# Performance work log

Measured on AMD Instinct MI355X. Metric: run time of the kernel, lower is better.

## Reference

```python
import jax, jax.numpy as jnp
import numpy as np

B, S, IN, OUT = 4, 2048, 4096, 4096

def setup_inputs() -> dict:
    key = jax.random.key(0)
    k1, k2, k3, k4 = jax.random.split(key, 4)
    x = jax.random.normal(k1, (B, S, IN), dtype=jnp.float32)
    # sign is mathematically +/-1 (sign of original fp weights)
    sign = jnp.sign(jax.random.normal(k2, (OUT, IN), dtype=jnp.float32))
    # per-row scale = mean(|W|), strictly positive
    scale = jax.random.uniform(k3, (OUT,), dtype=jnp.float32, minval=1e-3, maxval=0.1)
    bias = jax.random.normal(k4, (OUT,), dtype=jnp.float32)
    return {"x": x, "sign": sign, "scale": scale, "bias": bias}

def reference(x, sign, scale, bias) -> jnp.ndarray:
    # y = (x @ sign.T) * scale + bias  -- W approx diag(scale) * sign(W_orig)
    y = jnp.einsum('bsi,oi->bso', x, sign)
    return y * scale + bias
```

## Files before the change

### kernel.cpp

```cpp
#include <hip/hip_runtime.h>

#define M_DIM 8192
#define N_DIM 4096
#define K_DIM 4096
#define BK 32
#define NT (K_DIM / BK)

typedef __attribute__((ext_vector_type(8))) short bf16x8;
typedef __attribute__((ext_vector_type(8))) unsigned short u16x8;
typedef __attribute__((ext_vector_type(4))) float f32x4;

__device__ inline unsigned short f32_to_bf16_rne(float f) {
  unsigned int u = __float_as_uint(f);
  u += 0x7FFFu + ((u >> 16) & 1u);
  return (unsigned short)(u >> 16);
}

__global__ __launch_bounds__(256) void cvt_f32_bf16_kernel(
    const float* __restrict__ in, unsigned short* __restrict__ out) {
  const int i = (blockIdx.x * 256 + threadIdx.x) * 8;
  float4 v0 = *(const float4*)(in + i);
  float4 v1 = *(const float4*)(in + i + 4);
  u16x8 o;
  o[0] = f32_to_bf16_rne(v0.x);
  o[1] = f32_to_bf16_rne(v0.y);
  o[2] = f32_to_bf16_rne(v0.z);
  o[3] = f32_to_bf16_rne(v0.w);
  o[4] = f32_to_bf16_rne(v1.x);
  o[5] = f32_to_bf16_rne(v1.y);
  o[6] = f32_to_bf16_rne(v1.z);
  o[7] = f32_to_bf16_rne(v1.w);
  *(u16x8*)(out + i) = o;
}

__device__ inline void gld_lds16(const void* g, void* l) {
  __builtin_amdgcn_global_load_lds(
      (__attribute__((address_space(1))) void*)(g),
      (__attribute__((address_space(3))) void*)(l),
      16, 0, 0);
}

__global__ __launch_bounds__(512, 2) void gemm_sign_kernel(
    const unsigned short* __restrict__ A,
    const unsigned short* __restrict__ Bm,
    const float* __restrict__ scale,
    const float* __restrict__ bias,
    float* __restrict__ C) {
  __shared__ __align__(16) unsigned short smA[4][256 * BK];
  __shared__ __align__(16) unsigned short smB[4][256 * BK];

  const int tid   = threadIdx.x;
  const int lane  = tid & 63;
  const int wave  = tid >> 6;
  const int waveM = wave >> 2;
  const int waveN = wave & 3;
  const int lrow  = lane & 15;

  const int bid   = blockIdx.x;
  const int wgid  = (bid & 7) * 64 + (bid >> 3);
  const int mBase = (wgid >> 4) * 256;
  const int nBase = (wgid & 15) * 256;

  const int srow = tid >> 2;
  const int gcol = ((tid & 3) ^ ((tid >> 3) & 3)) * 8;
  const unsigned short* aSrc = A  + (size_t)(mBase + srow) * K_DIM + gcol;
  const unsigned short* bSrc = Bm + (size_t)(nBase + srow) * K_DIM + gcol;
  const size_t rowStr128 = (size_t)128 * K_DIM;

#define STAGE_A(buf, kt) do {                                        \
    const unsigned short* _s = aSrc + (size_t)(kt) * BK;             \
    gld_lds16(_s,             &smA[buf][tid * 8]);                   \
    gld_lds16(_s + rowStr128, &smA[buf][4096 + tid * 8]);            \
  } while (0)
#define STAGE_B(buf, kt) do {                                        \
    const unsigned short* _s = bSrc + (size_t)(kt) * BK;             \
    gld_lds16(_s,             &smB[buf][tid * 8]);                   \
    gld_lds16(_s + rowStr128, &smB[buf][4096 + tid * 8]);            \
  } while (0)

  const int cSwz = ((lane >> 4) ^ ((lrow >> 1) & 3)) * 8;
  int aOff[8], bOff[4];
#pragma unroll
  for (int mi = 0; mi < 8; ++mi)
    aOff[mi] = (waveM * 128 + mi * 16 + lrow) * BK + cSwz;
#pragma unroll
  for (int ni = 0; ni < 4; ++ni)
    bOff[ni] = (waveN * 64 + ni * 16 + lrow) * BK + cSwz;

  f32x4 acc[8][4];
#pragma unroll
  for (int i = 0; i < 8; ++i)
#pragma unroll
    for (int j = 0; j < 4; ++j)
      acc[i][j] = (f32x4){0.f, 0.f, 0.f, 0.f};

  STAGE_A(0, 0); STAGE_B(0, 0);
  STAGE_A(1, 1); STAGE_B(1, 1);
  asm volatile("s_waitcnt vmcnt(4)" ::: "memory");
  __builtin_amdgcn_s_barrier();

#pragma unroll 4
  for (int t = 0; t < NT; ++t) {
    const int cur = t & 3;
    const int pre = (t + 2) & 3;
    const int kt2 = (t + 2 < NT) ? (t + 2) : (NT - 1);
    bf16x8 af[4], bf[4];

#pragma unroll
    for (int ni = 0; ni < 4; ++ni)
      bf[ni] = *(const bf16x8*)&smB[cur][bOff[ni]];
#pragma unroll
    for (int mi = 0; mi < 4; ++mi)
      af[mi] = *(const bf16x8*)&smA[cur][aOff[mi]];
    STAGE_A(pre, kt2);
    __builtin_amdgcn_s_barrier();
    asm volatile("s_waitcnt lgkmcnt(0)" ::: "memory");
    __builtin_amdgcn_s_setprio(1);
#pragma unroll
    for (int mi = 0; mi < 4; ++mi)
#pragma unroll
      for (int ni = 0; ni < 4; ++ni)
        acc[mi][ni] = __builtin_amdgcn_mfma_f32_16x16x32_bf16(
            af[mi], bf[ni], acc[mi][ni], 0, 0, 0);
    __builtin_amdgcn_s_setprio(0);
    __builtin_amdgcn_s_barrier();

#pragma unroll
    for (int mi = 0; mi < 4; ++mi)
      af[mi] = *(const bf16x8*)&smA[cur][aOff[4 + mi]];
    STAGE_B(pre, kt2);
    asm volatile("s_waitcnt vmcnt(4)" ::: "memory");
    __builtin_amdgcn_s_barrier();
    asm volatile("s_waitcnt lgkmcnt(0)" ::: "memory");
    __builtin_amdgcn_s_setprio(1);
#pragma unroll
    for (int mi = 0; mi < 4; ++mi)
#pragma unroll
      for (int ni = 0; ni < 4; ++ni)
        acc[4 + mi][ni] = __builtin_amdgcn_mfma_f32_16x16x32_bf16(
            af[mi], bf[ni], acc[4 + mi][ni], 0, 0, 0);
    __builtin_amdgcn_s_setprio(0);
    __builtin_amdgcn_s_barrier();
  }
#undef STAGE_A
#undef STAGE_B

#pragma unroll
  for (int ni = 0; ni < 4; ++ni) {
    const int c = nBase + waveN * 64 + ni * 16 + lrow;
    const float sc = scale[c];
    const float bs = bias[c];
#pragma unroll
    for (int mi = 0; mi < 8; ++mi) {
      const int r0 = mBase + waveM * 128 + mi * 16 + (lane >> 4) * 4;
#pragma unroll
      for (int r = 0; r < 4; ++r)
        C[(size_t)(r0 + r) * N_DIM + c] = acc[mi][ni][r] * sc + bs;
    }
  }
}

extern "C" void kernel_launch(void* const* d_in, const int* in_sizes, int n_in,
                              void* d_out, int out_size, void* d_ws, size_t ws_size,
                              hipStream_t stream) {
  const float* x     = (const float*)d_in[0];
  const float* sign  = (const float*)d_in[1];
  const float* scale = (const float*)d_in[2];
  const float* bias  = (const float*)d_in[3];
  float* out = (float*)d_out;

  unsigned short* xb    = (unsigned short*)d_ws;
  unsigned short* signb = xb + (size_t)M_DIM * K_DIM;

  cvt_f32_bf16_kernel<<<(M_DIM * K_DIM) / 2048, 256, 0, stream>>>(x, xb);
  cvt_f32_bf16_kernel<<<(N_DIM * K_DIM) / 2048, 256, 0, stream>>>(sign, signb);

  gemm_sign_kernel<<<dim3(512), dim3(512), 0, stream>>>(xb, signb, scale, bias, out);
}
```

Measured before the change: 527.3 us.

## Deepen GEMM pipeline: prefetch three tiles and software-pipeline LDS fragment reads

The global-to-LDS prefetch distance goes from two to three K-tiles across the 4-slot ring. The main loop is software-pipelined so the next tile's A and B register fragments are read from LDS during the current tile's second MFMA half, using ping-pong B registers and partial lgkmcnt waits. The aim is to overlap LDS read latency and global load latency with MFMA work and to drop one barrier per half-step. In exchange it needs more registers and depends on delicate waitcnt and barrier ordering, where a mistake would cause a race.

```diff
diff --git a/kernel.cpp b/kernel.cpp
--- a/kernel.cpp
+++ b/kernel.cpp
@@ -94,54 +94,70 @@
     for (int j = 0; j < 4; ++j)
       acc[i][j] = (f32x4){0.f, 0.f, 0.f, 0.f};
 
+  bf16x8 afP[4], afQ[4], bfE[4], bfO[4];
+
   STAGE_A(0, 0); STAGE_B(0, 0);
   STAGE_A(1, 1); STAGE_B(1, 1);
+  STAGE_A(2, 2); STAGE_B(2, 2);
   asm volatile("s_waitcnt vmcnt(4)" ::: "memory");
   __builtin_amdgcn_s_barrier();
+#pragma unroll
+  for (int ni = 0; ni < 4; ++ni)
+    bfE[ni] = *(const bf16x8*)&smB[0][bOff[ni]];
+#pragma unroll
+  for (int mi = 0; mi < 4; ++mi)
+    afP[mi] = *(const bf16x8*)&smA[0][aOff[mi]];
 
-#pragma unroll 4
-  for (int t = 0; t < NT; ++t) {
-    const int cur = t & 3;
-    const int pre = (t + 2) & 3;
-    const int kt2 = (t + 2 < NT) ? (t + 2) : (NT - 1);
-    bf16x8 af[4], bf[4];
+#define TILE_BODY(t, bfC, bfN)                                          \
+  {                                                                     \
+    const int cur = (t) & 3;                                            \
+    const int pre = ((t) + 3) & 3;                                      \
+    const int kt3 = ((t) + 3 < NT) ? ((t) + 3) : (NT - 1);              \
+    const int ktn = ((t) + 1 < NT) ? ((t) + 1) : (NT - 1);              \
+    const int nxt = ktn & 3;                                            \
+        \
+    \
+    _Pragma("unroll")                                                   \
+    for (int mi = 0; mi < 4; ++mi)                                      \
+      afQ[mi] = *(const bf16x8*)&smA[cur][aOff[4 + mi]];                \
+    STAGE_A(pre, kt3);                                                  \
+    asm volatile("s_waitcnt lgkmcnt(4)" ::: "memory");                  \
+    __builtin_amdgcn_s_setprio(1);                                      \
+    _Pragma("unroll")                                                   \
+    for (int mi = 0; mi < 4; ++mi)                                      \
+      _Pragma("unroll")                                                 \
+      for (int ni = 0; ni < 4; ++ni)                                    \
+        acc[mi][ni] = __builtin_amdgcn_mfma_f32_16x16x32_bf16(          \
+            afP[mi], bfC[ni], acc[mi][ni], 0, 0, 0);                    \
+    __builtin_amdgcn_s_setprio(0);                                      \
+    __builtin_amdgcn_s_barrier();                                       \
+       \
+       \
+    _Pragma("unroll")                                                   \
+    for (int ni = 0; ni < 4; ++ni)                                      \
+      bfN[ni] = *(const bf16x8*)&smB[nxt][bOff[ni]];                    \
+    _Pragma("unroll")                                                   \
+    for (int mi = 0; mi < 4; ++mi)                                      \
+      afP[mi] = *(const bf16x8*)&smA[nxt][aOff[mi]];                    \
+    STAGE_B(pre, kt3);                                                  \
+    asm volatile("s_waitcnt lgkmcnt(8)" ::: "memory");                  \
+    __builtin_amdgcn_s_setprio(1);                                      \
+    _Pragma("unroll")                                                   \
+    for (int mi = 0; mi < 4; ++mi)                                      \
+      _Pragma("unroll")                                                 \
+      for (int ni = 0; ni < 4; ++ni)                                    \
+        acc[4 + mi][ni] = __builtin_amdgcn_mfma_f32_16x16x32_bf16(      \
+            afQ[mi], bfC[ni], acc[4 + mi][ni], 0, 0, 0);                \
+    __builtin_amdgcn_s_setprio(0);                                      \
+    asm volatile("s_waitcnt vmcnt(4)" ::: "memory");                    \
+    __builtin_amdgcn_s_barrier();                                       \
+  }
 
-#pragma unroll
-    for (int ni = 0; ni < 4; ++ni)
-      bf[ni] = *(const bf16x8*)&smB[cur][bOff[ni]];
-#pragma unroll
-    for (int mi = 0; mi < 4; ++mi)
-      af[mi] = *(const bf16x8*)&smA[cur][aOff[mi]];
-    STAGE_A(pre, kt2);
-    __builtin_amdgcn_s_barrier();
-    asm volatile("s_waitcnt lgkmcnt(0)" ::: "memory");
-    __builtin_amdgcn_s_setprio(1);
-#pragma unroll
-    for (int mi = 0; mi < 4; ++mi)
-#pragma unroll
-      for (int ni = 0; ni < 4; ++ni)
-        acc[mi][ni] = __builtin_amdgcn_mfma_f32_16x16x32_bf16(
-            af[mi], bf[ni], acc[mi][ni], 0, 0, 0);
-    __builtin_amdgcn_s_setprio(0);
-    __builtin_amdgcn_s_barrier();
-
-#pragma unroll
-    for (int mi = 0; mi < 4; ++mi)
-      af[mi] = *(const bf16x8*)&smA[cur][aOff[4 + mi]];
-    STAGE_B(pre, kt2);
-    asm volatile("s_waitcnt vmcnt(4)" ::: "memory");
-    __builtin_amdgcn_s_barrier();
-    asm volatile("s_waitcnt lgkmcnt(0)" ::: "memory");
-    __builtin_amdgcn_s_setprio(1);
-#pragma unroll
-    for (int mi = 0; mi < 4; ++mi)
-#pragma unroll
-      for (int ni = 0; ni < 4; ++ni)
-        acc[4 + mi][ni] = __builtin_amdgcn_mfma_f32_16x16x32_bf16(
-            af[mi], bf[ni], acc[4 + mi][ni], 0, 0, 0);
-    __builtin_amdgcn_s_setprio(0);
-    __builtin_amdgcn_s_barrier();
+  for (int t = 0; t < NT; t += 2) {
+    TILE_BODY(t,     bfE, bfO);
+    TILE_BODY(t + 1, bfO, bfE);
   }
+#undef TILE_BODY
 #undef STAGE_A
 #undef STAGE_B
 
```

New measurement: 523.8 us. No clear change (-0.7%).
